# Kernel tuning notes

Hardware: AMD Instinct MI355X
Metric: run time of the kernel (lower is better)

## Reference

```python
import jax, jax.numpy as jnp
import numpy as np

N_NODES = 50000
N_EDGES = 800000


def setup_inputs() -> dict:
    key = jax.random.key(0)
    ks = jax.random.split(key, 10)
    x = jax.random.normal(ks[0], (N_NODES, 256), dtype=jnp.float32)
    edge_index = jax.random.randint(ks[1], (2, N_EDGES), 0, N_NODES, dtype=jnp.int64)
    edge_attr = jax.random.uniform(ks[2], (N_EDGES,), dtype=jnp.float32)
    def glorot(k, fan_in, fan_out):
        s = jnp.sqrt(6.0 / (fan_in + fan_out))
        return jax.random.uniform(k, (fan_in, fan_out), minval=-s, maxval=s, dtype=jnp.float32)
    W1 = glorot(ks[3], 256, 512); b1 = jnp.zeros((512,), jnp.float32)
    W2 = glorot(ks[4], 512, 256); b2 = jnp.zeros((256,), jnp.float32)
    W3 = glorot(ks[5], 256, 128); b3 = jnp.zeros((128,), jnp.float32)
    return {"x": x, "edge_index": edge_index, "edge_attr": edge_attr,
            "W1": W1, "b1": b1, "W2": W2, "b2": b2, "W3": W3, "b3": b3}


def _gcn_norm(edge_index, edge_attr, num_nodes):
    # PyG GCNConv default: add self-loops (weight 1), symmetric normalization.
    loops = jnp.arange(num_nodes, dtype=edge_index.dtype)
    src = jnp.concatenate([edge_index[0], loops])
    dst = jnp.concatenate([edge_index[1], loops])
    w = jnp.concatenate([edge_attr, jnp.ones((num_nodes,), edge_attr.dtype)])
    deg = jax.ops.segment_sum(w, dst, num_segments=num_nodes)
    dinv = jnp.where(deg > 0, jax.lax.rsqrt(deg), 0.0)
    norm = dinv[src] * w * dinv[dst]  # [E+N]
    return src, dst, norm


def _gcn_conv(h, W, b, src, dst, norm, num_nodes):
    h = h @ W                                   # [N, Dout] linear transform
    msg = h[src] * norm[:, None]                # gather + per-edge scale
    out = jax.ops.segment_sum(msg, dst, num_segments=num_nodes)  # scatter-add
    return out + b


def reference(x, edge_index, edge_attr, W1, b1, W2, b2, W3, b3):
    src, dst, norm = _gcn_norm(edge_index, edge_attr, N_NODES)
    h = jax.nn.relu(_gcn_conv(x, W1, b1, src, dst, norm, N_NODES))
    # dropout is identity in eval mode (reference runs with training=False)
    h = jax.nn.relu(_gcn_conv(h, W2, b2, src, dst, norm, N_NODES))
    h = _gcn_conv(h, W3, b3, src, dst, norm, N_NODES)
    return h.reshape(-1, h.shape[1])
```

## Files before the change

kernel.cpp:

```cpp
#include <hip/hip_runtime.h>
#include <cstdint>
#include <cstddef>

typedef unsigned short u16;
typedef unsigned int u32;

#define NN 50000
#define NE 800000

typedef __attribute__((ext_vector_type(8))) short bf16x8;
typedef __attribute__((ext_vector_type(4))) float f32x4;

__device__ __forceinline__ u16 f2bf(float f) {
  union { float f; u32 i; } v; v.f = f;
  return (u16)((v.i + 0x7FFFu + ((v.i >> 16) & 1u)) >> 16);
}
__device__ __forceinline__ void bf2x2(u32 w, float& a, float& b) {
  union { u32 i; float f; } lo, hi;
  lo.i = w << 16; hi.i = w & 0xFFFF0000u;
  a = lo.f; b = hi.f;
}
__device__ __forceinline__ void unpack8(const uint4& q, float* f) {
  bf2x2(q.x, f[0], f[1]); bf2x2(q.y, f[2], f[3]);
  bf2x2(q.z, f[4], f[5]); bf2x2(q.w, f[6], f[7]);
}

__global__ void k_hist(int* __restrict__ cnt, const int* __restrict__ dst, int E) {
  int e = blockIdx.x * 256 + threadIdx.x;
  if (e < E) atomicAdd(&cnt[dst[e]], 1);
}
__global__ void k_scan_part(const int* __restrict__ cnt, int* __restrict__ bsum, int n) {
  __shared__ int s[256];
  int i = blockIdx.x * 256 + threadIdx.x;
  s[threadIdx.x] = (i < n) ? cnt[i] : 0;
  __syncthreads();
  for (int o = 128; o > 0; o >>= 1) {
    if (threadIdx.x < o) s[threadIdx.x] += s[threadIdx.x + o];
    __syncthreads();
  }
  if (threadIdx.x == 0) bsum[blockIdx.x] = s[0];
}
__global__ void k_scan_mid(const int* __restrict__ bsum, int* __restrict__ bpre, int nb) {
  if (blockIdx.x == 0 && threadIdx.x == 0) {
    int run = 0;
    for (int i = 0; i < nb; i++) { bpre[i] = run; run += bsum[i]; }
  }
}
__global__ void k_scan_fin(const int* __restrict__ cnt, const int* __restrict__ bpre,
                           int* __restrict__ rowptr, int* __restrict__ cursor, int n) {
  __shared__ int s[256];
  int i = blockIdx.x * 256 + threadIdx.x;
  s[threadIdx.x] = (i < n) ? cnt[i] : 0;
  __syncthreads();
  if (threadIdx.x == 0) {
    int run = bpre[blockIdx.x];
    for (int j = 0; j < 256; j++) { int t = s[j]; s[j] = run; run += t; }
  }
  __syncthreads();
  if (i < n) { rowptr[i] = s[threadIdx.x]; cursor[i] = s[threadIdx.x]; }
}
__global__ void k_fill(const int* __restrict__ src, const int* __restrict__ dst,
                       const float* __restrict__ w,
                       int* __restrict__ cursor, uint2* __restrict__ edges, int E) {
  int e = blockIdx.x * 256 + threadIdx.x;
  if (e < E) {
    int d = dst[e];
    int p = atomicAdd(&cursor[d], 1);
    uint2 ev;
    ev.x = (u32)src[e];
    ev.y = __float_as_uint(w[e]);
    edges[p] = ev;
  }
}

__global__ __launch_bounds__(256) void k_sortrow(
    uint2* __restrict__ edges, const int* __restrict__ rowptr,
    const int* __restrict__ cnt, float* __restrict__ dinv, int n) {
  int wave = threadIdx.x >> 6, lane = threadIdx.x & 63;
  int row = blockIdx.x * 4 + wave;
  if (row >= n) return;
  int p = rowptr[row], c = cnt[row];
  if (c <= 64) {
    u32 kc = 0xFFFFFFFFu, kw = 0xFFFFFFFFu;
    if (lane < c) { uint2 e = edges[p + lane]; kc = e.x; kw = e.y; }
#pragma unroll
    for (int k = 2; k <= 64; k <<= 1) {
#pragma unroll
      for (int j = k >> 1; j > 0; j >>= 1) {
        u32 oc = __shfl_xor(kc, j, 64);
        u32 ow = __shfl_xor(kw, j, 64);
        bool up = ((lane & k) == 0);
        bool lower = ((lane & j) == 0);
        bool gt = (kc > oc) || (kc == oc && kw > ow);
        bool lt = (kc < oc) || (kc == oc && kw < ow);
        bool swap = up ? (lower ? gt : lt) : (lower ? lt : gt);
        if (swap) { kc = oc; kw = ow; }
      }
    }
    float s = (lane < c) ? __uint_as_float(kw) : 0.f;
#pragma unroll
    for (int off = 1; off < 64; off <<= 1) s += __shfl_xor(s, off, 64);
    if (lane < c) { uint2 e; e.x = kc; e.y = kw; edges[p + lane] = e; }
    if (lane == 0) dinv[row] = rsqrtf(1.0f + s);
  } else {
    if (lane == 0) {
      for (int i = 1; i < c; i++) {
        uint2 key = edges[p + i];
        int j2 = i - 1;
        while (j2 >= 0) {
          uint2 a = edges[p + j2];
          bool gt = (a.x > key.x) || (a.x == key.x && a.y > key.y);
          if (!gt) break;
          edges[p + j2 + 1] = a; j2--;
        }
        edges[p + j2 + 1] = key;
      }
      float s = 0.f;
      for (int i = 0; i < c; i++) s += __uint_as_float(edges[p + i].y);
      dinv[row] = rsqrtf(1.0f + s);
    }
  }
}

__global__ __launch_bounds__(256) void k_val(
    uint2* __restrict__ edges, const int* __restrict__ rowptr,
    const int* __restrict__ cnt, const float* __restrict__ dinv, int n) {
  int wave = threadIdx.x >> 6, lane = threadIdx.x & 63;
  int row = blockIdx.x * 4 + wave;
  if (row >= n) return;
  int p = rowptr[row], c = cnt[row];
  float dr = dinv[row];
  for (int l = lane; l < c; l += 64) {
    uint2 e = edges[p + l];
    float w = __uint_as_float(e.y);
    e.y = __float_as_uint(dinv[(int)e.x] * w * dr);
    edges[p + l] = e;
  }
}

__global__ void k_castx(u16* __restrict__ o, const float* __restrict__ in, int n4) {
  int i = blockIdx.x * 256 + threadIdx.x;
  if (i < n4) {
    float4 f = ((const float4*)in)[i];
    uint2 u;
    u.x = (u32)f2bf(f.x) | ((u32)f2bf(f.y) << 16);
    u.y = (u32)f2bf(f.z) | ((u32)f2bf(f.w) << 16);
    ((uint2*)o)[i] = u;
  }
}
__global__ void k_wcast3(const float* __restrict__ W1, const float* __restrict__ W2,
                         const float* __restrict__ W3, u16* __restrict__ Wt1,
                         u16* __restrict__ Wt2, u16* __restrict__ Wt3) {
  int i = blockIdx.x * 256 + threadIdx.x;
  if (i < 131072) {
    int k = i >> 9, n = i & 511;
    Wt1[n * 256 + k] = f2bf(W1[i]);
  } else if (i < 262144) {
    int j = i - 131072;
    int k = j >> 8, n = j & 255;
    Wt2[n * 512 + k] = f2bf(W2[j]);
  } else if (i < 294912) {
    int j = i - 262144;
    int k = j >> 7, n = j & 127;
    Wt3[n * 256 + k] = f2bf(W3[j]);
  }
}

template <int D, int OUTF32, int RELU, int HASB, int U>
__global__ __launch_bounds__(128) void k_agg(
    const u16* __restrict__ H, const int* __restrict__ rowptr,
    const int* __restrict__ cnt, const uint2* __restrict__ edges,
    const float* __restrict__ dinv,
    const float* __restrict__ bias, void* __restrict__ outv) {
  constexpr int RL = D / 8;
  constexpr int EPW = 64 / RL;
  int wave = threadIdx.x >> 6, lane = threadIdx.x & 63;
  int node = blockIdx.x * 2 + wave;
  if (node >= NN) return;
  const int sub = lane / RL;
  const int rl = lane & (RL - 1);
  const int base = rl * 8;
  float acc[8] = {};
  if (sub == 0) {
    float dv = dinv[node];
    float sw = dv * dv;
    uint4 q = *(const uint4*)(H + (size_t)node * D + base);
    float f[8]; unpack8(q, f);
#pragma unroll
    for (int j = 0; j < 8; j++) acc[j] = sw * f[j];
  }
  const int p = rowptr[node], c = cnt[node];
  for (int e0 = 0; e0 < c; e0 += EPW * U) {
    uint4 q[U];
    float v[U];
#pragma unroll
    for (int u = 0; u < U; u++) {
      int id = e0 + sub + u * EPW;
      bool ok = id < c;
      uint2 ev = edges[p + (ok ? id : 0)];
      v[u] = ok ? __uint_as_float(ev.y) : 0.f;
      int cs = ok ? (int)ev.x : node;
      q[u] = *(const uint4*)(H + (size_t)cs * D + base);
    }
#pragma unroll
    for (int u = 0; u < U; u++) {
      float f[8]; unpack8(q[u], f);
#pragma unroll
      for (int j = 0; j < 8; j++) acc[j] += v[u] * f[j];
    }
  }
#pragma unroll
  for (int j = 0; j < 8; j++) {
#pragma unroll
    for (int off = RL; off < 64; off <<= 1)
      acc[j] += __shfl_xor(acc[j], off, 64);
  }
  if (sub == 0) {
#pragma unroll
    for (int j = 0; j < 8; j++) {
      float v2 = acc[j];
      if (HASB) v2 += bias[base + j];
      if (RELU) v2 = fmaxf(v2, 0.f);
      acc[j] = v2;
    }
    if (OUTF32) {
      float* o = (float*)outv + (size_t)node * D + base;
      float4 f0 = {acc[0], acc[1], acc[2], acc[3]};
      float4 f1 = {acc[4], acc[5], acc[6], acc[7]};
      *(float4*)o = f0;
      *(float4*)(o + 4) = f1;
    } else {
      u16* o = (u16*)outv + (size_t)node * D + base;
      uint4 u;
      u.x = (u32)f2bf(acc[0]) | ((u32)f2bf(acc[1]) << 16);
      u.y = (u32)f2bf(acc[2]) | ((u32)f2bf(acc[3]) << 16);
      u.z = (u32)f2bf(acc[4]) | ((u32)f2bf(acc[5]) << 16);
      u.w = (u32)f2bf(acc[6]) | ((u32)f2bf(acc[7]) << 16);
      *(uint4*)o = u;
    }
  }
}

template <int RELU, int HASB>
__global__ __launch_bounds__(256) void k_gemm(
    const u16* __restrict__ A, const u16* __restrict__ Bt,
    const float* __restrict__ bias, u16* __restrict__ C, int M, int Nd, int K) {
  __shared__ u16 As[128 * 64];
  __shared__ u16 Bs[128 * 64];
  const int tid = threadIdx.x;
  const int wave = tid >> 6, lane = tid & 63;
  const int m0 = blockIdx.x * 128, n0 = blockIdx.y * 128;
  const int wr = wave >> 1, wc = wave & 1;
  f32x4 acc[4][4] = {};

  for (int k0 = 0; k0 < K; k0 += 64) {
#pragma unroll
    for (int i = 0; i < 4; i++) {
      int r = i * 32 + wave * 8 + (lane >> 3);
      int rg = m0 + r; rg = rg < M ? rg : M - 1;
      const u16* ga = A + (size_t)rg * K + k0 + (lane & 7) * 8;
      __builtin_amdgcn_global_load_lds(
          (const __attribute__((address_space(1))) void*)ga,
          (__attribute__((address_space(3))) void*)&As[(i * 32 + wave * 8) * 64], 16, 0, 0);
      int ng = n0 + r;
      const u16* gb = Bt + (size_t)ng * K + k0 + (lane & 7) * 8;
      __builtin_amdgcn_global_load_lds(
          (const __attribute__((address_space(1))) void*)gb,
          (__attribute__((address_space(3))) void*)&Bs[(i * 32 + wave * 8) * 64], 16, 0, 0);
    }
    __syncthreads();
#pragma unroll
    for (int kk = 0; kk < 2; kk++) {
      bf16x8 af[4], bfr[4];
#pragma unroll
      for (int mi = 0; mi < 4; mi++)
        af[mi] = *(const bf16x8*)&As[(wr * 64 + mi * 16 + (lane & 15)) * 64 + kk * 32 + (lane >> 4) * 8];
#pragma unroll
      for (int ni = 0; ni < 4; ni++)
        bfr[ni] = *(const bf16x8*)&Bs[(wc * 64 + ni * 16 + (lane & 15)) * 64 + kk * 32 + (lane >> 4) * 8];
#pragma unroll
      for (int mi = 0; mi < 4; mi++)
#pragma unroll
        for (int ni = 0; ni < 4; ni++)
          acc[mi][ni] = __builtin_amdgcn_mfma_f32_16x16x32_bf16(af[mi], bfr[ni], acc[mi][ni], 0, 0, 0);
    }
    __syncthreads();
  }
  const int nb = n0 + wc * 64 + (lane & 15);
  float bv[4];
#pragma unroll
  for (int ni = 0; ni < 4; ni++) bv[ni] = HASB ? bias[nb + ni * 16] : 0.f;
#pragma unroll
  for (int mi = 0; mi < 4; mi++) {
#pragma unroll
    for (int r = 0; r < 4; r++) {
      int row = m0 + wr * 64 + mi * 16 + (lane >> 4) * 4 + r;
      if (row < M) {
#pragma unroll
        for (int ni = 0; ni < 4; ni++) {
          float v = acc[mi][ni][r] + bv[ni];
          if (RELU) v = fmaxf(v, 0.f);
          C[(size_t)row * Nd + nb + ni * 16] = f2bf(v);
        }
      }
    }
  }
}

extern "C" void kernel_launch(void* const* d_in, const int* in_sizes, int n_in,
                              void* d_out, int out_size, void* d_ws, size_t ws_size,
                              hipStream_t stream) {
  const float* x  = (const float*)d_in[0];
  const int*   ei = (const int*)d_in[1];
  const float* ea = (const float*)d_in[2];
  const float* W1 = (const float*)d_in[3];
  const float* b1 = (const float*)d_in[4];
  const float* W2 = (const float*)d_in[5];
  const float* b2 = (const float*)d_in[6];
  const float* W3 = (const float*)d_in[7];
  const float* b3 = (const float*)d_in[8];
  const int* e_src = ei;
  const int* e_dst = ei + NE;

  size_t off = 0;
  auto carve = [&](size_t bytes) -> void* {
    void* r = (char*)d_ws + off;
    off += (bytes + 255) & ~(size_t)255;
    return r;
  };
  float* dinv   = (float*)carve(NN * 4);
  int*   counts = (int*)carve(NN * 4);
  int*   rowptr = (int*)carve(NN * 4);
  int*   cursor = (int*)carve(NN * 4);
  int*   bsum   = (int*)carve(256 * 4);
  int*   bpre   = (int*)carve(256 * 4);
  uint2* edges  = (uint2*)carve((size_t)NE * 8);
  u16*   Wt1    = (u16*)carve(512 * 256 * 2);
  u16*   Wt2    = (u16*)carve(256 * 512 * 2);
  u16*   Wt3    = (u16*)carve(128 * 256 * 2);
  u16*   R0     = (u16*)carve((size_t)NN * 256 * 2);
  u16*   R1     = (u16*)carve((size_t)NN * 256 * 2);
  u16*   R2     = (u16*)carve((size_t)NN * 512 * 2);

  const int NB_N = (NN + 255) / 256;
  const int NB_E = (NE + 255) / 256;
  const int ROW_B = (NN + 3) / 4;
  const int AGG_B = (NN + 1) / 2;

  hipMemsetAsync(counts, 0, (size_t)NN * 4, stream);
  k_hist<<<NB_E, 256, 0, stream>>>(counts, e_dst, NE);
  k_scan_part<<<NB_N, 256, 0, stream>>>(counts, bsum, NN);
  k_scan_mid<<<1, 64, 0, stream>>>(bsum, bpre, NB_N);
  k_scan_fin<<<NB_N, 256, 0, stream>>>(counts, bpre, rowptr, cursor, NN);
  k_fill<<<NB_E, 256, 0, stream>>>(e_src, e_dst, ea, cursor, edges, NE);
  k_sortrow<<<ROW_B, 256, 0, stream>>>(edges, rowptr, counts, dinv, NN);
  k_val<<<ROW_B, 256, 0, stream>>>(edges, rowptr, counts, dinv, NN);

  k_castx<<<(NN * 256 / 4 + 255) / 256, 256, 0, stream>>>(R0, x, NN * 256 / 4);
  k_wcast3<<<(294912 + 255) / 256, 256, 0, stream>>>(W1, W2, W3, Wt1, Wt2, Wt3);

  dim3 g1((NN + 127) / 128, 512 / 128);
  dim3 g2((NN + 127) / 128, 256 / 128);
  dim3 g3((NN + 127) / 128, 128 / 128);

  k_agg<256, 0, 0, 0, 4><<<AGG_B, 128, 0, stream>>>(R0, rowptr, counts, edges, dinv, nullptr, R1);
  k_gemm<1, 1><<<g1, 256, 0, stream>>>(R1, Wt1, b1, R2, NN, 512, 256);
  k_gemm<0, 0><<<g2, 256, 0, stream>>>(R2, Wt2, nullptr, R0, NN, 256, 512);
  k_agg<256, 0, 1, 1, 4><<<AGG_B, 128, 0, stream>>>(R0, rowptr, counts, edges, dinv, b2, R1);
  k_gemm<0, 0><<<g3, 256, 0, stream>>>(R1, Wt3, nullptr, R0, NN, 128, 256);
  k_agg<128, 1, 0, 1, 4><<<AGG_B, 128, 0, stream>>>(R0, rowptr, counts, edges, dinv, b3, d_out);
}
```

Before: 415.2 us.

## Fold scan-mid into scan-fin, merge cast kernels, enlarge GEMM tile to 256 rows

Removes the single-thread k_scan_mid launch: each k_scan_fin block now tree-reduces the preceding block sums itself. Merges the x cast and weight transpose-cast into one launch. Grows the GEMM block to 512 threads and 256 output rows, so the B tile is reused across twice as many rows. That cuts launch overhead and B-tile reloads, at the cost of more LDS and larger blocks that may lower occupancy.

```diff
diff --git a/kernel.cpp b/kernel.cpp
--- a/kernel.cpp
+++ b/kernel.cpp
@@ -40,24 +40,25 @@
   }
   if (threadIdx.x == 0) bsum[blockIdx.x] = s[0];
 }
-__global__ void k_scan_mid(const int* __restrict__ bsum, int* __restrict__ bpre, int nb) {
-  if (blockIdx.x == 0 && threadIdx.x == 0) {
-    int run = 0;
-    for (int i = 0; i < nb; i++) { bpre[i] = run; run += bsum[i]; }
-  }
-}
-__global__ void k_scan_fin(const int* __restrict__ cnt, const int* __restrict__ bpre,
+__global__ void k_scan_fin(const int* __restrict__ cnt, const int* __restrict__ bsum,
                            int* __restrict__ rowptr, int* __restrict__ cursor, int n) {
   __shared__ int s[256];
-  int i = blockIdx.x * 256 + threadIdx.x;
-  s[threadIdx.x] = (i < n) ? cnt[i] : 0;
+  __shared__ int pre[256];
+  int t = threadIdx.x;
+  int i = blockIdx.x * 256 + t;
+  pre[t] = (t < blockIdx.x) ? bsum[t] : 0;
+  s[t] = (i < n) ? cnt[i] : 0;
   __syncthreads();
-  if (threadIdx.x == 0) {
-    int run = bpre[blockIdx.x];
-    for (int j = 0; j < 256; j++) { int t = s[j]; s[j] = run; run += t; }
+  for (int o = 128; o > 0; o >>= 1) {
+    if (t < o) pre[t] += pre[t + o];
+    __syncthreads();
+  }
+  if (t == 0) {
+    int run = pre[0];
+    for (int j = 0; j < 256; j++) { int v = s[j]; s[j] = run; run += v; }
   }
   __syncthreads();
-  if (i < n) { rowptr[i] = s[threadIdx.x]; cursor[i] = s[threadIdx.x]; }
+  if (i < n) { rowptr[i] = s[t]; cursor[i] = s[t]; }
 }
 __global__ void k_fill(const int* __restrict__ src, const int* __restrict__ dst,
                        const float* __restrict__ w,
@@ -138,31 +139,32 @@
   }
 }
 
-__global__ void k_castx(u16* __restrict__ o, const float* __restrict__ in, int n4) {
+#define XGROUPS (NN * 256 / 4)
+__global__ void k_cast_all(const float* __restrict__ x, const float* __restrict__ W1,
+                           const float* __restrict__ W2, const float* __restrict__ W3,
+                           u16* __restrict__ xb, u16* __restrict__ Wt1,
+                           u16* __restrict__ Wt2, u16* __restrict__ Wt3) {
   int i = blockIdx.x * 256 + threadIdx.x;
-  if (i < n4) {
-    float4 f = ((const float4*)in)[i];
+  if (i < XGROUPS) {
+    float4 f = ((const float4*)x)[i];
     uint2 u;
     u.x = (u32)f2bf(f.x) | ((u32)f2bf(f.y) << 16);
     u.y = (u32)f2bf(f.z) | ((u32)f2bf(f.w) << 16);
-    ((uint2*)o)[i] = u;
-  }
-}
-__global__ void k_wcast3(const float* __restrict__ W1, const float* __restrict__ W2,
-                         const float* __restrict__ W3, u16* __restrict__ Wt1,
-                         u16* __restrict__ Wt2, u16* __restrict__ Wt3) {
-  int i = blockIdx.x * 256 + threadIdx.x;
-  if (i < 131072) {
-    int k = i >> 9, n = i & 511;
-    Wt1[n * 256 + k] = f2bf(W1[i]);
-  } else if (i < 262144) {
-    int j = i - 131072;
-    int k = j >> 8, n = j & 255;
-    Wt2[n * 512 + k] = f2bf(W2[j]);
-  } else if (i < 294912) {
-    int j = i - 262144;
-    int k = j >> 7, n = j & 127;
-    Wt3[n * 256 + k] = f2bf(W3[j]);
+    ((uint2*)xb)[i] = u;
+  } else {
+    int j = i - XGROUPS;
+    if (j < 131072) {
+      int k = j >> 9, n = j & 511;
+      Wt1[n * 256 + k] = f2bf(W1[j]);
+    } else if (j < 262144) {
+      int j2 = j - 131072;
+      int k = j2 >> 8, n = j2 & 255;
+      Wt2[n * 512 + k] = f2bf(W2[j2]);
+    } else if (j < 294912) {
+      int j2 = j - 262144;
+      int k = j2 >> 7, n = j2 & 127;
+      Wt3[n * 256 + k] = f2bf(W3[j2]);
+    }
   }
 }
 
@@ -242,31 +244,35 @@
 }
 
 template <int RELU, int HASB>
-__global__ __launch_bounds__(256) void k_gemm(
+__global__ __launch_bounds__(512) void k_gemm(
     const u16* __restrict__ A, const u16* __restrict__ Bt,
     const float* __restrict__ bias, u16* __restrict__ C, int M, int Nd, int K) {
-  __shared__ u16 As[128 * 64];
+  __shared__ u16 As[256 * 64];
   __shared__ u16 Bs[128 * 64];
   const int tid = threadIdx.x;
   const int wave = tid >> 6, lane = tid & 63;
-  const int m0 = blockIdx.x * 128, n0 = blockIdx.y * 128;
+  const int m0 = blockIdx.x * 256, n0 = blockIdx.y * 128;
   const int wr = wave >> 1, wc = wave & 1;
   f32x4 acc[4][4] = {};
 
   for (int k0 = 0; k0 < K; k0 += 64) {
 #pragma unroll
     for (int i = 0; i < 4; i++) {
-      int r = i * 32 + wave * 8 + (lane >> 3);
+      int r = i * 64 + wave * 8 + (lane >> 3);
       int rg = m0 + r; rg = rg < M ? rg : M - 1;
       const u16* ga = A + (size_t)rg * K + k0 + (lane & 7) * 8;
       __builtin_amdgcn_global_load_lds(
           (const __attribute__((address_space(1))) void*)ga,
-          (__attribute__((address_space(3))) void*)&As[(i * 32 + wave * 8) * 64], 16, 0, 0);
+          (__attribute__((address_space(3))) void*)&As[(i * 64 + wave * 8) * 64], 16, 0, 0);
+    }
+#pragma unroll
+    for (int i = 0; i < 2; i++) {
+      int r = i * 64 + wave * 8 + (lane >> 3);
       int ng = n0 + r;
       const u16* gb = Bt + (size_t)ng * K + k0 + (lane & 7) * 8;
       __builtin_amdgcn_global_load_lds(
           (const __attribute__((address_space(1))) void*)gb,
-          (__attribute__((address_space(3))) void*)&Bs[(i * 32 + wave * 8) * 64], 16, 0, 0);
+          (__attribute__((address_space(3))) void*)&Bs[(i * 64 + wave * 8) * 64], 16, 0, 0);
     }
     __syncthreads();
 #pragma unroll
@@ -333,7 +339,6 @@
   int*   rowptr = (int*)carve(NN * 4);
   int*   cursor = (int*)carve(NN * 4);
   int*   bsum   = (int*)carve(256 * 4);
-  int*   bpre   = (int*)carve(256 * 4);
   uint2* edges  = (uint2*)carve((size_t)NE * 8);
   u16*   Wt1    = (u16*)carve(512 * 256 * 2);
   u16*   Wt2    = (u16*)carve(256 * 512 * 2);
@@ -350,23 +355,22 @@
   hipMemsetAsync(counts, 0, (size_t)NN * 4, stream);
   k_hist<<<NB_E, 256, 0, stream>>>(counts, e_dst, NE);
   k_scan_part<<<NB_N, 256, 0, stream>>>(counts, bsum, NN);
-  k_scan_mid<<<1, 64, 0, stream>>>(bsum, bpre, NB_N);
-  k_scan_fin<<<NB_N, 256, 0, stream>>>(counts, bpre, rowptr, cursor, NN);
+  k_scan_fin<<<NB_N, 256, 0, stream>>>(counts, bsum, rowptr, cursor, NN);
   k_fill<<<NB_E, 256, 0, stream>>>(e_src, e_dst, ea, cursor, edges, NE);
   k_sortrow<<<ROW_B, 256, 0, stream>>>(edges, rowptr, counts, dinv, NN);
   k_val<<<ROW_B, 256, 0, stream>>>(edges, rowptr, counts, dinv, NN);
 
-  k_castx<<<(NN * 256 / 4 + 255) / 256, 256, 0, stream>>>(R0, x, NN * 256 / 4);
-  k_wcast3<<<(294912 + 255) / 256, 256, 0, stream>>>(W1, W2, W3, Wt1, Wt2, Wt3);
-
-  dim3 g1((NN + 127) / 128, 512 / 128);
-  dim3 g2((NN + 127) / 128, 256 / 128);
-  dim3 g3((NN + 127) / 128, 128 / 128);
+  k_cast_all<<<(XGROUPS + 294912 + 255) / 256, 256, 0, stream>>>(
+      x, W1, W2, W3, R0, Wt1, Wt2, Wt3);
+
+  dim3 g1((NN + 255) / 256, 512 / 128);
+  dim3 g2((NN + 255) / 256, 256 / 128);
+  dim3 g3((NN + 255) / 256, 128 / 128);
 
   k_agg<256, 0, 0, 0, 4><<<AGG_B, 128, 0, stream>>>(R0, rowptr, counts, edges, dinv, nullptr, R1);
-  k_gemm<1, 1><<<g1, 256, 0, stream>>>(R1, Wt1, b1, R2, NN, 512, 256);
-  k_gemm<0, 0><<<g2, 256, 0, stream>>>(R2, Wt2, nullptr, R0, NN, 256, 512);
+  k_gemm<1, 1><<<g1, 512, 0, stream>>>(R1, Wt1, b1, R2, NN, 512, 256);
+  k_gemm<0, 0><<<g2, 512, 0, stream>>>(R2, Wt2, nullptr, R0, NN, 256, 512);
   k_agg<256, 0, 1, 1, 4><<<AGG_B, 128, 0, stream>>>(R0, rowptr, counts, edges, dinv, b2, R1);
-  k_gemm<0, 0><<<g3, 256, 0, stream>>>(R1, Wt3, nullptr, R0, NN, 128, 256);
+  k_gemm<0, 0><<<g3, 512, 0, stream>>>(R1, Wt3, nullptr, R0, NN, 128, 256);
   k_agg<128, 1, 0, 1, 4><<<AGG_B, 128, 0, stream>>>(R0, rowptr, counts, edges, dinv, b3, d_out);
 }
```

Result: faster. 391.0 us (-5.8%).
